# Performance work log

Measured on AMD Instinct MI355X. Metric: run time of the kernel, lower is better.

The kernel has to match this reference:

```python
import jax, jax.numpy as jnp
import numpy as np

MODES = 16
WIDTH = 64
DEPTH = 4
MLP = 128


def spectral_conv(x, w_cplx):
    # x: [B, C, H, W] float32; w_cplx: [C, C, m1, m2] complex64
    B, C, H, W = x.shape
    x_ft = jnp.fft.rfft2(x)  # [B, C, H, W//2+1] complex
    m1, m2 = MODES, MODES
    low = jnp.einsum('bixy,ioxy->boxy', x_ft[:, :, :m1, :m2], w_cplx)
    out_ft = jnp.zeros((B, C, H, W // 2 + 1), dtype=jnp.complex64)
    out_ft = out_ft.at[:, :, :m1, :m2].set(low)
    return jnp.fft.irfft2(out_ft, s=(H, W)).astype(x.dtype)


def conv1x1(x, w, b):
    # x: [B,Cin,H,W], w: [Cout,Cin], b: [Cout]
    return jnp.einsum('bihw,oi->bohw', x, w) + b[None, :, None, None]


def setup_inputs() -> dict:
    key = jax.random.key(0)
    ks = jax.random.split(key, 4 + 4 * DEPTH)
    inp = {}
    inp['x'] = jax.random.normal(ks[0], (8, 3, 256, 256), dtype=jnp.float32)
    inp['fc0_w'] = jax.random.normal(ks[1], (WIDTH, 3), dtype=jnp.float32) * 0.1
    inp['fc0_b'] = jnp.zeros((WIDTH,), dtype=jnp.float32)
    scale = 1.0 / (WIDTH * WIDTH)
    sw_re, sw_im, ww, wb = [], [], [], []
    for i in range(DEPTH):
        k1, k2, k3 = jax.random.split(ks[4 + i], 3)
        sw_re.append(scale * jax.random.uniform(k1, (WIDTH, WIDTH, MODES, MODES), dtype=jnp.float32))
        sw_im.append(scale * jax.random.uniform(k2, (WIDTH, WIDTH, MODES, MODES), dtype=jnp.float32))
        ww.append(jax.random.normal(k3, (WIDTH, WIDTH), dtype=jnp.float32) * 0.05)
        wb.append(jnp.zeros((WIDTH,), dtype=jnp.float32))
    inp['spec_w_re'] = jnp.stack(sw_re)  # [D, C, C, m1, m2]
    inp['spec_w_im'] = jnp.stack(sw_im)
    inp['w_w'] = jnp.stack(ww)           # [D, C, C]
    inp['w_b'] = jnp.stack(wb)           # [D, C]
    inp['fc1_w'] = jax.random.normal(ks[2], (MLP, WIDTH), dtype=jnp.float32) * 0.05
    inp['fc1_b'] = jnp.zeros((MLP,), dtype=jnp.float32)
    inp['fc2_w'] = jax.random.normal(ks[3], (3, MLP), dtype=jnp.float32) * 0.05
    inp['fc2_b'] = jnp.zeros((3,), dtype=jnp.float32)
    return inp


def reference(x, fc0_w, fc0_b, spec_w_re, spec_w_im, w_w, w_b, fc1_w, fc1_b, fc2_w, fc2_b):
    # Dropout is identity in eval mode.
    h = conv1x1(x, fc0_w, fc0_b)  # [B, WIDTH, H, W]
    for i in range(DEPTH):
        w_cplx = spec_w_re[i] + 1j * spec_w_im[i]
        x1 = spectral_conv(h, w_cplx)
        x2 = conv1x1(h, w_w[i], w_b[i])
        h = jax.nn.relu(x1 + x2)
    h = jnp.transpose(h, (0, 2, 3, 1))  # [B, H, W, WIDTH]
    h = jax.nn.relu(jnp.einsum('bhwc,mc->bhwm', h, fc1_w) + fc1_b)
    h = jnp.einsum('bhwm,om->bhwo', h, fc2_w) + fc2_b
    return jnp.transpose(h, (0, 3, 1, 2))  # [B, 3, H, W]
```

## Files before the change

### kernel.cpp

```cpp
#include <hip/hip_runtime.h>

#define Hd 256
#define Wd 256
#define HW 65536
#define C 64
#define B 8
#define M 16
#define NDEPTH 4
#define NMLP 128

typedef __attribute__((ext_vector_type(8))) __bf16 bf16x8;
typedef __attribute__((ext_vector_type(4))) float f32x4;

__device__ inline void bar_lgkm() {
    asm volatile("s_waitcnt lgkmcnt(0)" ::: "memory");
    __builtin_amdgcn_s_barrier();
}

__device__ inline void split_pack8(const float* v, uint4& hq, uint4& lq) {
    unsigned hw[4], lw[4];
#pragma unroll
    for (int i = 0; i < 4; ++i) {
        float a = v[2 * i], bb = v[2 * i + 1];
        unsigned ua = __float_as_uint(a);
        unsigned ha = (ua + 0x7fffu + ((ua >> 16) & 1u)) & 0xffff0000u;
        float ra = a - __uint_as_float(ha);
        unsigned ural = __float_as_uint(ra);
        unsigned la = (ural + 0x7fffu + ((ural >> 16) & 1u)) >> 16;
        unsigned ub = __float_as_uint(bb);
        unsigned hb = (ub + 0x7fffu + ((ub >> 16) & 1u)) & 0xffff0000u;
        float rb = bb - __uint_as_float(hb);
        unsigned urbl = __float_as_uint(rb);
        unsigned lb = (urbl + 0x7fffu + ((urbl >> 16) & 1u)) >> 16;
        hw[i] = (ha >> 16) | (hb & 0xffff0000u);
        lw[i] = la | (lb << 16);
    }
    hq = make_uint4(hw[0], hw[1], hw[2], hw[3]);
    lq = make_uint4(lw[0], lw[1], lw[2], lw[3]);
}

__device__ inline void split1(float s, ushort& h, ushort& l) {
    unsigned ua = __float_as_uint(s);
    unsigned ha = (ua + 0x7fffu + ((ua >> 16) & 1u)) & 0xffff0000u;
    float r = s - __uint_as_float(ha);
    unsigned ur = __float_as_uint(r);
    h = (ushort)(ha >> 16);
    l = (ushort)((ur + 0x7fffu + ((ur >> 16) & 1u)) >> 16);
}

__device__ inline uint4 pack8(const unsigned* v) {
    uint4 r;
    r.x = v[0] | (v[1] << 16);
    r.y = v[2] | (v[3] << 16);
    r.z = v[4] | (v[5] << 16);
    r.w = v[6] | (v[7] << 16);
    return r;
}


__global__ void k_table(float2* __restrict__ tab) {
    int t = threadIdx.x;
    double a = (6.283185307179586476925286766559 / 256.0) * (double)t;
    tab[t] = make_float2((float)cos(a), (float)sin(a));
}

__global__ void k_prep0(const float2* __restrict__ tab, const float* __restrict__ fc1w,
                        const float* __restrict__ ww, float* __restrict__ trig,
                        uint4* __restrict__ trigs_h, uint4* __restrict__ trigs_l,
                        uint4* __restrict__ wws_h, uint4* __restrict__ wws_l,
                        uint4* __restrict__ w1s_h, uint4* __restrict__ w1s_l) {
    int blk = blockIdx.x, t = threadIdx.x;
    if (blk < 32) {
        int k = blk & 15;
        float2 e = tab[(k * t) & 255];
        trig[blk * 256 + t] = (blk < 16) ? e.x : e.y;
    } else if (blk < 36) {
        int idx = (blk - 32) * 256 + t;
        int kc = idx >> 8, x = idx & 255;
        float v[8];
#pragma unroll
        for (int j = 0; j < 8; ++j) {
            int row = kc * 8 + j;
            float2 e = tab[((row & 15) * x) & 255];
            v[j] = (row < 16) ? e.x : e.y;
        }
        uint4 hq, lq; split_pack8(v, hq, lq);
        trigs_h[idx] = hq; trigs_l[idx] = lq;
    } else if (blk < 44) {
        int idx = (blk - 36) * 256 + t;
        int o = idx & 63, kc = (idx >> 6) & 3, ph = (idx >> 8) & 1, d = idx >> 9;
        float v[8];
#pragma unroll
        for (int j = 0; j < 8; ++j)
            v[j] = ww[d * 4096 + o * 64 + ph * 32 + kc * 8 + j];
        uint4 hq, lq; split_pack8(v, hq, lq);
        wws_h[idx] = hq; wws_l[idx] = lq;
    } else {
        int idx = (blk - 44) * 256 + t;
        int m = idx & 127, kc = (idx >> 7) & 3, ph = idx >> 9;
        float v[8];
#pragma unroll
        for (int j = 0; j < 8; ++j)
            v[j] = fc1w[m * 64 + ph * 32 + kc * 8 + j];
        uint4 hq, lq; split_pack8(v, hq, lq);
        w1s_h[idx] = hq; w1s_l[idx] = lq;
    }
}

__global__ void k_prep_et(const float2* __restrict__ tab,
                          uint4* __restrict__ ETh, uint4* __restrict__ ETl) {
    int c = blockIdx.x * 256 + threadIdx.x;
    if (c >= 1024) return;
    int ph = c >> 7, kc = (c >> 5) & 3, m = c & 31;
    float v[8];
#pragma unroll
    for (int j = 0; j < 8; ++j) {
        int y = ph * 32 + kc * 8 + j;
        float2 e = tab[((m & 15) * y) & 255];
        v[j] = (m < 16) ? e.x : -e.y;
    }
    uint4 hq, lq;
    split_pack8(v, hq, lq);
    ETh[c] = hq; ETl[c] = lq;
}

__global__ void k_fc0(const float* __restrict__ x, const float* __restrict__ w,
                      const float* __restrict__ bias,
                      ushort* __restrict__ hs_h, ushort* __restrict__ hs_l) {
    int gp = blockIdx.x * 256 + threadIdx.x;
    int b = gp >> 13, pg = gp & 8191;
    int pix0 = pg * 8;
    float xv[3][8];
#pragma unroll
    for (int ch = 0; ch < 3; ++ch) {
        float4 a = *(const float4*)(x + (size_t)(b * 3 + ch) * HW + pix0);
        float4 c4 = *(const float4*)(x + (size_t)(b * 3 + ch) * HW + pix0 + 4);
        xv[ch][0] = a.x; xv[ch][1] = a.y; xv[ch][2] = a.z; xv[ch][3] = a.w;
        xv[ch][4] = c4.x; xv[ch][5] = c4.y; xv[ch][6] = c4.z; xv[ch][7] = c4.w;
    }
    for (int o = 0; o < C; ++o) {
        float w0 = w[o * 3 + 0], w1 = w[o * 3 + 1], w2 = w[o * 3 + 2], bv = bias[o];
        float v[8];
#pragma unroll
        for (int j = 0; j < 8; ++j)
            v[j] = fmaf(w0, xv[0][j], fmaf(w1, xv[1][j], fmaf(w2, xv[2][j], bv)));
        uint4 hq, lq; split_pack8(v, hq, lq);
        *(uint4*)(hs_h + (size_t)(b * 64 + o) * HW + pix0) = hq;
        *(uint4*)(hs_l + (size_t)(b * 64 + o) * HW + pix0) = lq;
    }
}

__global__ __launch_bounds__(256, 4)
void k_fwd_y(const ushort* __restrict__ hs_h, const ushort* __restrict__ hs_l,
             const uint4* __restrict__ ETh, const uint4* __restrict__ ETl,
             float* __restrict__ T1F) {
    int blk = blockIdx.x;
    int xh = blk & 1, bc = blk >> 1;
    int x0 = xh * 128;
    int t = threadIdx.x;
    int w = t >> 6, l = t & 63;
    int lr = l & 15, lq = l >> 4;
    const ushort* pH = hs_h + (size_t)bc * HW + x0 + w * 32 + lr;
    const ushort* pL = hs_l + (size_t)bc * HW + x0 + w * 32 + lr;
    f32x4 acc[2][2];
#pragma unroll
    for (int u = 0; u < 2; ++u)
#pragma unroll
        for (int xt = 0; xt < 2; ++xt) {
            acc[u][xt][0] = 0.f; acc[u][xt][1] = 0.f;
            acc[u][xt][2] = 0.f; acc[u][xt][3] = 0.f;
        }
    unsigned h0[2][8], l0[2][8], h1[2][8], l1[2][8];
    auto loadp = [&](unsigned hv[2][8], unsigned lv[2][8], int ph) {
#pragma unroll
        for (int xt = 0; xt < 2; ++xt)
#pragma unroll
            for (int j = 0; j < 8; ++j) {
                int off = (ph * 32 + lq * 8 + j) * 256 + xt * 16;
                hv[xt][j] = pH[off];
                lv[xt][j] = pL[off];
            }
    };
    loadp(h0, l0, 0);
#pragma unroll
    for (int ph = 0; ph < 8; ++ph) {
        unsigned (*ch)[8] = (ph & 1) ? h1 : h0;
        unsigned (*cl)[8] = (ph & 1) ? l1 : l0;
        unsigned (*nh)[8] = (ph & 1) ? h0 : h1;
        unsigned (*nl)[8] = (ph & 1) ? l0 : l1;
        if (ph < 7) loadp(nh, nl, ph + 1);
        bf16x8 Ah[2], Al[2];
#pragma unroll
        for (int u = 0; u < 2; ++u) {
            int ci = ph * 128 + lq * 32 + u * 16 + lr;
            Ah[u] = __builtin_bit_cast(bf16x8, ETh[ci]);
            Al[u] = __builtin_bit_cast(bf16x8, ETl[ci]);
        }
#pragma unroll
        for (int xt = 0; xt < 2; ++xt) {
            bf16x8 Bh = __builtin_bit_cast(bf16x8, pack8(ch[xt]));
            bf16x8 Bl = __builtin_bit_cast(bf16x8, pack8(cl[xt]));
#pragma unroll
            for (int u = 0; u < 2; ++u) {
                acc[u][xt] = __builtin_amdgcn_mfma_f32_16x16x32_bf16(Ah[u], Bh, acc[u][xt], 0, 0, 0);
                acc[u][xt] = __builtin_amdgcn_mfma_f32_16x16x32_bf16(Ah[u], Bl, acc[u][xt], 0, 0, 0);
                acc[u][xt] = __builtin_amdgcn_mfma_f32_16x16x32_bf16(Al[u], Bh, acc[u][xt], 0, 0, 0);
            }
        }
    }
#pragma unroll
    for (int u = 0; u < 2; ++u)
#pragma unroll
        for (int xt = 0; xt < 2; ++xt)
#pragma unroll
            for (int g = 0; g < 4; ++g)
                T1F[(size_t)bc * 8192 + (u * 16 + lq * 4 + g) * 256 + x0 + w * 32 + xt * 16 + lr] =
                    acc[u][xt][g];
}

__global__ __launch_bounds__(256, 2)
void k_fwd_x(const float* __restrict__ T1F, const float* __restrict__ trig,
             float2* __restrict__ X) {
    __shared__ float sT[32 * 260];
    __shared__ float sG[32 * 260];
    int bc = blockIdx.x, t = threadIdx.x;
#pragma unroll
    for (int p = 0; p < 8; ++p) {
        int f = t + p * 256;
        int row = f >> 6, seg = f & 63;
        ((float4*)(sT + row * 260))[seg] = *(const float4*)(T1F + (size_t)bc * 8192 + f * 4);
        ((float4*)(sG + row * 260))[seg] = *(const float4*)(trig + row * 256 + seg * 4);
    }
    __syncthreads();
    int ky = t >> 4, kx = t & 15;
    const float* Tr = sT + ky * 260;
    const float* Ti = sT + (16 + ky) * 260;
    const float* Cs = sG + kx * 260;
    const float* Sn = sG + (16 + kx) * 260;
    float xr0 = 0.f, xi0 = 0.f, xr1 = 0.f, xi1 = 0.f;
    for (int q = 0; q < 64; q += 2) {
        float4 tr = *(const float4*)(Tr + q * 4);
        float4 ti = *(const float4*)(Ti + q * 4);
        float4 cs = *(const float4*)(Cs + q * 4);
        float4 sn = *(const float4*)(Sn + q * 4);
        xr0 = fmaf(tr.x, cs.x, xr0); xr0 = fmaf(ti.x, sn.x, xr0);
        xi0 = fmaf(ti.x, cs.x, xi0); xi0 = fmaf(-tr.x, sn.x, xi0);
        xr0 = fmaf(tr.y, cs.y, xr0); xr0 = fmaf(ti.y, sn.y, xr0);
        xi0 = fmaf(ti.y, cs.y, xi0); xi0 = fmaf(-tr.y, sn.y, xi0);
        xr0 = fmaf(tr.z, cs.z, xr0); xr0 = fmaf(ti.z, sn.z, xr0);
        xi0 = fmaf(ti.z, cs.z, xi0); xi0 = fmaf(-tr.z, sn.z, xi0);
        xr0 = fmaf(tr.w, cs.w, xr0); xr0 = fmaf(ti.w, sn.w, xr0);
        xi0 = fmaf(ti.w, cs.w, xi0); xi0 = fmaf(-tr.w, sn.w, xi0);
        float4 tr1 = *(const float4*)(Tr + q * 4 + 4);
        float4 ti1 = *(const float4*)(Ti + q * 4 + 4);
        float4 cs1 = *(const float4*)(Cs + q * 4 + 4);
        float4 sn1 = *(const float4*)(Sn + q * 4 + 4);
        xr1 = fmaf(tr1.x, cs1.x, xr1); xr1 = fmaf(ti1.x, sn1.x, xr1);
        xi1 = fmaf(ti1.x, cs1.x, xi1); xi1 = fmaf(-tr1.x, sn1.x, xi1);
        xr1 = fmaf(tr1.y, cs1.y, xr1); xr1 = fmaf(ti1.y, sn1.y, xr1);
        xi1 = fmaf(ti1.y, cs1.y, xi1); xi1 = fmaf(-tr1.y, sn1.y, xi1);
        xr1 = fmaf(tr1.z, cs1.z, xr1); xr1 = fmaf(ti1.z, sn1.z, xr1);
        xi1 = fmaf(ti1.z, cs1.z, xi1); xi1 = fmaf(-tr1.z, sn1.z, xi1);
        xr1 = fmaf(tr1.w, cs1.w, xr1); xr1 = fmaf(ti1.w, sn1.w, xr1);
        xi1 = fmaf(ti1.w, cs1.w, xi1); xi1 = fmaf(-tr1.w, sn1.w, xi1);
    }
    X[bc * 256 + t] = make_float2(xr0 + xr1, xi0 + xi1);
}

__global__ __launch_bounds__(256, 2)
void k_mix(const float2* __restrict__ X, const float* __restrict__ wre,
           const float* __restrict__ wim, float2* __restrict__ Y) {
    int o = blockIdx.x >> 2;
    int bq = blockIdx.x & 3;
    int m = threadIdx.x;
    int b0 = bq * 2, b1 = bq * 2 + 1;
    float yr0 = 0.f, yi0 = 0.f, yr1 = 0.f, yi1 = 0.f;
    for (int i = 0; i < C; ++i) {
        float wr = wre[(i * C + o) * 256 + m];
        float wi = wim[(i * C + o) * 256 + m];
        float2 x0 = X[(b0 * C + i) * 256 + m];
        float2 x1 = X[(b1 * C + i) * 256 + m];
        yr0 = fmaf(x0.x, wr, fmaf(-x0.y, wi, yr0));
        yi0 = fmaf(x0.x, wi, fmaf(x0.y, wr, yi0));
        yr1 = fmaf(x1.x, wr, fmaf(-x1.y, wi, yr1));
        yi1 = fmaf(x1.x, wi, fmaf(x1.y, wr, yi1));
    }
    Y[(b0 * C + o) * 256 + m] = make_float2(yr0, yi0);
    Y[(b1 * C + o) * 256 + m] = make_float2(yr1, yi1);
}

__global__ __launch_bounds__(256, 2)
void k_invy(const float2* __restrict__ Y, const float2* __restrict__ tab,
            float* __restrict__ Gq) {
    __shared__ float2 st[256];
    int blk = blockIdx.x;
    int yt = blk & 15, pg = (blk >> 4) & 3, b = blk >> 6;
    int t = threadIdx.x;
    st[t] = tab[t];
    int o = t & 63, kx = pg * 4 + (t >> 6);
    __syncthreads();
    float sc = (kx == 0 ? 1.0f : 2.0f) * (1.0f / 65536.0f);
    float yr[16], yi[16];
    const float2* yp = Y + (size_t)(b * 64 + o) * 256 + kx;
#pragma unroll
    for (int ky = 0; ky < 16; ++ky) {
        float2 v = yp[ky * 16];
        yr[ky] = v.x * sc;
        yi[ky] = v.y * sc;
    }
    int y0 = yt * 16;
    for (int yy = 0; yy < 16; ++yy) {
        int y = y0 + yy;
        float re = 0.f, im = 0.f;
#pragma unroll
        for (int ky = 0; ky < 16; ++ky) {
            float2 e = st[(ky * y) & 255];
            re = fmaf(yr[ky], e.x, re);
            re = fmaf(-yi[ky], e.y, re);
            im = fmaf(yr[ky], e.y, im);
            im = fmaf(yi[ky], e.x, im);
        }
        float* gp = Gq + (size_t)(b * 256 + y) * 32 * 64 + o;
        gp[kx * 64] = re;
        gp[(16 + kx) * 64] = -im;
    }
}

__global__ __launch_bounds__(256, 4)
void k_final(ushort* __restrict__ hs_h, ushort* __restrict__ hs_l,
             const float* __restrict__ Gq,
             const uint4* __restrict__ wws_h, const uint4* __restrict__ wws_l,
             const float* __restrict__ wb,
             const uint4* __restrict__ trigs_h, const uint4* __restrict__ trigs_l) {
    __shared__ uint4 smem[2560];
    uint4* sH0h = smem;
    uint4* sH0l = smem + 512;
    uint4* sH1h = smem + 1024;
    uint4* sH1l = smem + 1536;
    uint4* sGh  = smem + 2048;
    uint4* sGl  = smem + 2304;
    int blk = blockIdx.x;
    int xq = blk & 1, y = (blk >> 1) & 255, b = blk >> 9;
    int x0 = xq * 128;
    int t = threadIdx.x;
    int os = t & 63, q = t >> 6;
    int w = t >> 6, l = t & 63;
    int lr = l & 15, lq = l >> 4;
    int xs = t & 127, half = t >> 7;
    f32x4 acc[8];
    {
        int ob = w * 16 + lq * 4;
        f32x4 ini;
        ini[0] = wb[ob]; ini[1] = wb[ob + 1]; ini[2] = wb[ob + 2]; ini[3] = wb[ob + 3];
#pragma unroll
        for (int xt = 0; xt < 8; ++xt) acc[xt] = ini;
    }
    float gv[8];
    {
        const float* gsrc = Gq + ((size_t)(b * 256 + y) * 32 + q * 8) * 64 + os;
#pragma unroll
        for (int kk = 0; kk < 8; ++kk) gv[kk] = gsrc[kk * 64];
    }
    uint4 A0h = wws_h[lq * 64 + w * 16 + lr];
    uint4 A0l = wws_l[lq * 64 + w * 16 + lr];
    uint4 A1h = wws_h[(4 + lq) * 64 + w * 16 + lr];
    uint4 A1l = wws_l[(4 + lq) * 64 + w * 16 + lr];
    size_t hb0 = (size_t)(b * 64 + half * 16) * HW + y * 256 + x0 + xs;
    unsigned hv[16], lv[16];
#pragma unroll
    for (int j = 0; j < 16; ++j) {
        hv[j] = hs_h[hb0 + (size_t)j * HW];
        lv[j] = hs_l[hb0 + (size_t)j * HW];
    }
    {
        uint4 ghq, glq; split_pack8(gv, ghq, glq);
        sGh[q * 64 + os] = ghq; sGl[q * 64 + os] = glq;
    }
#pragma unroll
    for (int c2 = 0; c2 < 2; ++c2) {
        int cell = (half * 2 + c2) * 128 + xs;
        sH0h[cell] = pack8(hv + c2 * 8);
        sH0l[cell] = pack8(lv + c2 * 8);
    }
    unsigned hv1[16], lv1[16];
    size_t hb1 = hb0 + (size_t)32 * HW;
#pragma unroll
    for (int j = 0; j < 16; ++j) {
        hv1[j] = hs_h[hb1 + (size_t)j * HW];
        lv1[j] = hs_l[hb1 + (size_t)j * HW];
    }
    bar_lgkm();
#pragma unroll
    for (int xt = 0; xt < 8; ++xt) {
        bf16x8 Bh = __builtin_bit_cast(bf16x8, sH0h[lq * 128 + xt * 16 + lr]);
        bf16x8 Bl = __builtin_bit_cast(bf16x8, sH0l[lq * 128 + xt * 16 + lr]);
        bf16x8 Ah = __builtin_bit_cast(bf16x8, A0h);
        bf16x8 Al = __builtin_bit_cast(bf16x8, A0l);
        acc[xt] = __builtin_amdgcn_mfma_f32_16x16x32_bf16(Ah, Bh, acc[xt], 0, 0, 0);
        acc[xt] = __builtin_amdgcn_mfma_f32_16x16x32_bf16(Ah, Bl, acc[xt], 0, 0, 0);
        acc[xt] = __builtin_amdgcn_mfma_f32_16x16x32_bf16(Al, Bh, acc[xt], 0, 0, 0);
    }
#pragma unroll
    for (int c2 = 0; c2 < 2; ++c2) {
        int cell = (half * 2 + c2) * 128 + xs;
        sH1h[cell] = pack8(hv1 + c2 * 8);
        sH1l[cell] = pack8(lv1 + c2 * 8);
    }
    bar_lgkm();
#pragma unroll
    for (int xt = 0; xt < 8; ++xt) {
        bf16x8 Bh = __builtin_bit_cast(bf16x8, sH1h[lq * 128 + xt * 16 + lr]);
        bf16x8 Bl = __builtin_bit_cast(bf16x8, sH1l[lq * 128 + xt * 16 + lr]);
        bf16x8 Ah = __builtin_bit_cast(bf16x8, A1h);
        bf16x8 Al = __builtin_bit_cast(bf16x8, A1l);
        acc[xt] = __builtin_amdgcn_mfma_f32_16x16x32_bf16(Ah, Bh, acc[xt], 0, 0, 0);
        acc[xt] = __builtin_amdgcn_mfma_f32_16x16x32_bf16(Ah, Bl, acc[xt], 0, 0, 0);
        acc[xt] = __builtin_amdgcn_mfma_f32_16x16x32_bf16(Al, Bh, acc[xt], 0, 0, 0);
    }
    {
        bf16x8 Ah = __builtin_bit_cast(bf16x8, sGh[lq * 64 + w * 16 + lr]);
        bf16x8 Al = __builtin_bit_cast(bf16x8, sGl[lq * 64 + w * 16 + lr]);
#pragma unroll
        for (int xt = 0; xt < 8; ++xt) {
            bf16x8 Bh = __builtin_bit_cast(bf16x8, trigs_h[lq * 256 + x0 + xt * 16 + lr]);
            bf16x8 Bl = __builtin_bit_cast(bf16x8, trigs_l[lq * 256 + x0 + xt * 16 + lr]);
            acc[xt] = __builtin_amdgcn_mfma_f32_16x16x32_bf16(Ah, Bh, acc[xt], 0, 0, 0);
            acc[xt] = __builtin_amdgcn_mfma_f32_16x16x32_bf16(Ah, Bl, acc[xt], 0, 0, 0);
            acc[xt] = __builtin_amdgcn_mfma_f32_16x16x32_bf16(Al, Bh, acc[xt], 0, 0, 0);
        }
    }
    __syncthreads();
    ushort* eh = (ushort*)smem;
    ushort* el = (ushort*)(smem + 1024);
#pragma unroll
    for (int xt = 0; xt < 8; ++xt)
#pragma unroll
        for (int g = 0; g < 4; ++g) {
            int o = w * 16 + lq * 4 + g;
            float r = fmaxf(acc[xt][g], 0.f);
            ushort hh, ll; split1(r, hh, ll);
            eh[o * 128 + xt * 16 + lr] = hh;
            el[o * 128 + xt * 16 + lr] = ll;
        }
    __syncthreads();
#pragma unroll
    for (int p = 0; p < 4; ++p) {
        int f = t + p * 256;
        int o = f >> 4, seg = f & 15;
        size_t base = (size_t)(b * 64 + o) * HW + y * 256 + x0;
        *(uint4*)(hs_h + base + seg * 8) = smem[f];
        *(uint4*)(hs_l + base + seg * 8) = smem[1024 + f];
    }
}

__global__ __launch_bounds__(256, 3)
void k_fc12(const ushort* __restrict__ hs_h, const ushort* __restrict__ hs_l,
            const uint4* __restrict__ w1s_h, const uint4* __restrict__ w1s_l,
            const float* __restrict__ b1, const float* __restrict__ w2,
            const float* __restrict__ b2, float* __restrict__ out) {
    __shared__ uint4 sH0h[512], sH0l[512], sH1h[512], sH1l[512];
    int blk = blockIdx.x;
    int xq = blk & 1, y = (blk >> 1) & 255, b = blk >> 9;
    int x0 = xq * 128;
    int t = threadIdx.x;
    int w = t >> 6, l = t & 63;
    int lr = l & 15, lq = l >> 4;
    int mb = w * 32;
    int xs = t & 127, half = t >> 7;
    f32x4 acc[2][8];
#pragma unroll
    for (int u = 0; u < 2; ++u) {
        int m0 = mb + u * 16 + lq * 4;
        f32x4 ini;
        ini[0] = b1[m0]; ini[1] = b1[m0 + 1]; ini[2] = b1[m0 + 2]; ini[3] = b1[m0 + 3];
#pragma unroll
        for (int xt = 0; xt < 8; ++xt) acc[u][xt] = ini;
    }
    uint4 a0h[2], a0l[2], a1h[2], a1l[2];
#pragma unroll
    for (int u = 0; u < 2; ++u) {
        a0h[u] = w1s_h[lq * 128 + mb + u * 16 + lr];
        a0l[u] = w1s_l[lq * 128 + mb + u * 16 + lr];
        a1h[u] = w1s_h[(4 + lq) * 128 + mb + u * 16 + lr];
        a1l[u] = w1s_l[(4 + lq) * 128 + mb + u * 16 + lr];
    }
    size_t hb0 = (size_t)(b * 64 + half * 16) * HW + y * 256 + x0 + xs;
    unsigned hv[16], lv[16];
#pragma unroll
    for (int j = 0; j < 16; ++j) {
        hv[j] = hs_h[hb0 + (size_t)j * HW];
        lv[j] = hs_l[hb0 + (size_t)j * HW];
    }
#pragma unroll
    for (int c2 = 0; c2 < 2; ++c2) {
        int cell = (half * 2 + c2) * 128 + xs;
        sH0h[cell] = pack8(hv + c2 * 8);
        sH0l[cell] = pack8(lv + c2 * 8);
    }
    unsigned hv1[16], lv1[16];
    size_t hb1 = hb0 + (size_t)32 * HW;
#pragma unroll
    for (int j = 0; j < 16; ++j) {
        hv1[j] = hs_h[hb1 + (size_t)j * HW];
        lv1[j] = hs_l[hb1 + (size_t)j * HW];
    }
    bar_lgkm();
#pragma unroll
    for (int xt = 0; xt < 8; ++xt) {
        bf16x8 Bh = __builtin_bit_cast(bf16x8, sH0h[lq * 128 + xt * 16 + lr]);
        bf16x8 Bl = __builtin_bit_cast(bf16x8, sH0l[lq * 128 + xt * 16 + lr]);
#pragma unroll
        for (int u = 0; u < 2; ++u) {
            bf16x8 Ah = __builtin_bit_cast(bf16x8, a0h[u]);
            bf16x8 Al = __builtin_bit_cast(bf16x8, a0l[u]);
            acc[u][xt] = __builtin_amdgcn_mfma_f32_16x16x32_bf16(Ah, Bh, acc[u][xt], 0, 0, 0);
            acc[u][xt] = __builtin_amdgcn_mfma_f32_16x16x32_bf16(Ah, Bl, acc[u][xt], 0, 0, 0);
            acc[u][xt] = __builtin_amdgcn_mfma_f32_16x16x32_bf16(Al, Bh, acc[u][xt], 0, 0, 0);
        }
    }
#pragma unroll
    for (int c2 = 0; c2 < 2; ++c2) {
        int cell = (half * 2 + c2) * 128 + xs;
        sH1h[cell] = pack8(hv1 + c2 * 8);
        sH1l[cell] = pack8(lv1 + c2 * 8);
    }
    bar_lgkm();
#pragma unroll
    for (int xt = 0; xt < 8; ++xt) {
        bf16x8 Bh = __builtin_bit_cast(bf16x8, sH1h[lq * 128 + xt * 16 + lr]);
        bf16x8 Bl = __builtin_bit_cast(bf16x8, sH1l[lq * 128 + xt * 16 + lr]);
#pragma unroll
        for (int u = 0; u < 2; ++u) {
            bf16x8 Ah = __builtin_bit_cast(bf16x8, a1h[u]);
            bf16x8 Al = __builtin_bit_cast(bf16x8, a1l[u]);
            acc[u][xt] = __builtin_amdgcn_mfma_f32_16x16x32_bf16(Ah, Bh, acc[u][xt], 0, 0, 0);
            acc[u][xt] = __builtin_amdgcn_mfma_f32_16x16x32_bf16(Ah, Bl, acc[u][xt], 0, 0, 0);
            acc[u][xt] = __builtin_amdgcn_mfma_f32_16x16x32_bf16(Al, Bh, acc[u][xt], 0, 0, 0);
        }
    }
    float pj[3][8];
#pragma unroll
    for (int j = 0; j < 3; ++j)
#pragma unroll
        for (int xt = 0; xt < 8; ++xt) pj[j][xt] = 0.f;
#pragma unroll
    for (int u = 0; u < 2; ++u)
#pragma unroll
        for (int g = 0; g < 4; ++g) {
            int m = mb + u * 16 + lq * 4 + g;
            float w20 = w2[m], w21 = w2[NMLP + m], w22 = w2[2 * NMLP + m];
#pragma unroll
            for (int xt = 0; xt < 8; ++xt) {
                float r = fmaxf(acc[u][xt][g], 0.f);
                pj[0][xt] = fmaf(w20, r, pj[0][xt]);
                pj[1][xt] = fmaf(w21, r, pj[1][xt]);
                pj[2][xt] = fmaf(w22, r, pj[2][xt]);
            }
        }
#pragma unroll
    for (int j = 0; j < 3; ++j)
#pragma unroll
        for (int xt = 0; xt < 8; ++xt) {
            float v = pj[j][xt];
            v += __shfl_xor(v, 16);
            v += __shfl_xor(v, 32);
            pj[j][xt] = v;
        }
    float* part = (float*)sH0h;
    if (lq == 0) {
#pragma unroll
        for (int j = 0; j < 3; ++j)
#pragma unroll
            for (int xt = 0; xt < 8; ++xt)
                part[(w * 3 + j) * 128 + xt * 16 + lr] = pj[j][xt];
    }
    __syncthreads();
#pragma unroll
    for (int r = 0; r < 2; ++r) {
        int idx = t + r * 256;
        if (idx < 384) {
            int j = idx >> 7, xx = idx & 127;
            float s = b2[j];
#pragma unroll
            for (int ww2 = 0; ww2 < 4; ++ww2) s += part[(ww2 * 3 + j) * 128 + xx];
            out[(size_t)(b * 3 + j) * HW + y * 256 + x0 + xx] = s;
        }
    }
}

extern "C" void kernel_launch(void* const* d_in, const int* in_sizes, int n_in,
                              void* d_out, int out_size, void* d_ws, size_t ws_size,
                              hipStream_t stream) {
    const float* x     = (const float*)d_in[0];
    const float* fc0_w = (const float*)d_in[1];
    const float* fc0_b = (const float*)d_in[2];
    const float* swre  = (const float*)d_in[3];
    const float* swim  = (const float*)d_in[4];
    const float* ww    = (const float*)d_in[5];
    const float* wb    = (const float*)d_in[6];
    const float* fc1w  = (const float*)d_in[7];
    const float* fc1b  = (const float*)d_in[8];
    const float* fc2w  = (const float*)d_in[9];
    const float* fc2b  = (const float*)d_in[10];

    float* ws = (float*)d_ws;
    float2* tab     = (float2*)ws;
    ushort* hs_h    = (ushort*)(ws + 512);
    ushort* hs_l    = (ushort*)(ws + 512 + 16777216);
    float*  T1F     = ws + 33554944;
    float2* X       = (float2*)(ws + 37749248);
    float2* Y       = (float2*)(ws + 38011392);
    float*  Gq      = ws + 38273536;
    float*  trig    = ws + 42467840;
    uint4*  trigs_h = (uint4*)(ws + 42476032);
    uint4*  trigs_l = (uint4*)(ws + 42480128);
    uint4*  wws_h   = (uint4*)(ws + 42484224);
    uint4*  wws_l   = (uint4*)(ws + 42492416);
    uint4*  w1s_h   = (uint4*)(ws + 42500608);
    uint4*  w1s_l   = (uint4*)(ws + 42504704);
    uint4*  ETh     = (uint4*)(ws + 42508800);
    uint4*  ETl     = (uint4*)(ws + 42512896);

    k_table<<<dim3(1), dim3(256), 0, stream>>>(tab);
    k_prep0<<<dim3(48), dim3(256), 0, stream>>>(tab, fc1w, ww, trig,
                                                trigs_h, trigs_l, wws_h, wws_l,
                                                w1s_h, w1s_l);
    k_prep_et<<<dim3(4), dim3(256), 0, stream>>>(tab, ETh, ETl);
    k_fc0<<<dim3(256), dim3(256), 0, stream>>>(x, fc0_w, fc0_b, hs_h, hs_l);

    for (int d = 0; d < NDEPTH; ++d) {
        k_fwd_y<<<dim3(1024), dim3(256), 0, stream>>>(hs_h, hs_l, ETh, ETl, T1F);
        k_fwd_x<<<dim3(512), dim3(256), 0, stream>>>(T1F, trig, X);
        k_mix<<<dim3(256), dim3(256), 0, stream>>>(X, swre + (size_t)d * C * C * 256,
                                                   swim + (size_t)d * C * C * 256, Y);
        k_invy<<<dim3(512), dim3(256), 0, stream>>>(Y, tab, Gq);
        k_final<<<dim3(4096), dim3(256), 0, stream>>>(hs_h, hs_l, Gq,
                                                      wws_h + (size_t)d * 512,
                                                      wws_l + (size_t)d * 512,
                                                      wb + d * C, trigs_h, trigs_l);
    }
    k_fc12<<<dim3(4096), dim3(256), 0, stream>>>(hs_h, hs_l, w1s_h, w1s_l,
                                                 fc1b, fc2w, fc2b, (float*)d_out);
}
```

Baseline: 693.8 us.

## Fuse final spectral layer with fc1/fc2 head and trim k_final LDS

The last depth layer's output update is fused with the fc1/fc2 MLP head, so that layer's activations go from registers into LDS and straight into the fc1 MFMAs. This avoids writing the hs_h/hs_l tensors to global memory and reading them back in a separate k_fc12 launch. k_final also builds the G operand in registers instead of staging it through LDS, cutting LDS from 40KB to 32KB and raising the occupancy hint to 5 blocks. It adds an XOR swizzle on the epilogue LDS writes to reduce bank conflicts. The fused kernel carries more accumulator registers, which may limit its occupancy.

```diff
diff --git a/kernel.cpp b/kernel.cpp
--- a/kernel.cpp
+++ b/kernel.cpp
@@ -326,24 +326,21 @@
     }
 }
 
-__global__ __launch_bounds__(256, 4)
+__global__ __launch_bounds__(256, 5)
 void k_final(ushort* __restrict__ hs_h, ushort* __restrict__ hs_l,
              const float* __restrict__ Gq,
              const uint4* __restrict__ wws_h, const uint4* __restrict__ wws_l,
              const float* __restrict__ wb,
              const uint4* __restrict__ trigs_h, const uint4* __restrict__ trigs_l) {
-    __shared__ uint4 smem[2560];
+    __shared__ uint4 smem[2048];
     uint4* sH0h = smem;
     uint4* sH0l = smem + 512;
     uint4* sH1h = smem + 1024;
     uint4* sH1l = smem + 1536;
-    uint4* sGh  = smem + 2048;
-    uint4* sGl  = smem + 2304;
     int blk = blockIdx.x;
     int xq = blk & 1, y = (blk >> 1) & 255, b = blk >> 9;
     int x0 = xq * 128;
     int t = threadIdx.x;
-    int os = t & 63, q = t >> 6;
     int w = t >> 6, l = t & 63;
     int lr = l & 15, lq = l >> 4;
     int xs = t & 127, half = t >> 7;
@@ -357,7 +354,7 @@
     }
     float gv[8];
     {
-        const float* gsrc = Gq + ((size_t)(b * 256 + y) * 32 + q * 8) * 64 + os;
+        const float* gsrc = Gq + ((size_t)(b * 256 + y) * 32 + lq * 8) * 64 + w * 16 + lr;
 #pragma unroll
         for (int kk = 0; kk < 8; ++kk) gv[kk] = gsrc[kk * 64];
     }
@@ -371,10 +368,6 @@
     for (int j = 0; j < 16; ++j) {
         hv[j] = hs_h[hb0 + (size_t)j * HW];
         lv[j] = hs_l[hb0 + (size_t)j * HW];
-    }
-    {
-        uint4 ghq, glq; split_pack8(gv, ghq, glq);
-        sGh[q * 64 + os] = ghq; sGl[q * 64 + os] = glq;
     }
 #pragma unroll
     for (int c2 = 0; c2 < 2; ++c2) {
@@ -418,8 +411,9 @@
         acc[xt] = __builtin_amdgcn_mfma_f32_16x16x32_bf16(Al, Bh, acc[xt], 0, 0, 0);
     }
     {
-        bf16x8 Ah = __builtin_bit_cast(bf16x8, sGh[lq * 64 + w * 16 + lr]);
-        bf16x8 Al = __builtin_bit_cast(bf16x8, sGl[lq * 64 + w * 16 + lr]);
+        uint4 gh4, gl4; split_pack8(gv, gh4, gl4);
+        bf16x8 Ah = __builtin_bit_cast(bf16x8, gh4);
+        bf16x8 Al = __builtin_bit_cast(bf16x8, gl4);
 #pragma unroll
         for (int xt = 0; xt < 8; ++xt) {
             bf16x8 Bh = __builtin_bit_cast(bf16x8, trigs_h[lq * 256 + x0 + xt * 16 + lr]);
@@ -432,6 +426,7 @@
     __syncthreads();
     ushort* eh = (ushort*)smem;
     ushort* el = (ushort*)(smem + 1024);
+    int swz = lq * 40;
 #pragma unroll
     for (int xt = 0; xt < 8; ++xt)
 #pragma unroll
@@ -439,103 +434,168 @@
             int o = w * 16 + lq * 4 + g;
             float r = fmaxf(acc[xt][g], 0.f);
             ushort hh, ll; split1(r, hh, ll);
-            eh[o * 128 + xt * 16 + lr] = hh;
-            el[o * 128 + xt * 16 + lr] = ll;
+            int col = (xt * 16 + lr) ^ swz;
+            eh[o * 128 + col] = hh;
+            el[o * 128 + col] = ll;
         }
     __syncthreads();
 #pragma unroll
     for (int p = 0; p < 4; ++p) {
         int f = t + p * 256;
         int o = f >> 4, seg = f & 15;
+        int ko = ((o >> 2) & 3) * 40;
+        int cb = (seg * 8) ^ ko;
         size_t base = (size_t)(b * 64 + o) * HW + y * 256 + x0;
-        *(uint4*)(hs_h + base + seg * 8) = smem[f];
-        *(uint4*)(hs_l + base + seg * 8) = smem[1024 + f];
+        *(uint4*)(hs_h + base + seg * 8) = *(uint4*)(eh + o * 128 + cb);
+        *(uint4*)(hs_l + base + seg * 8) = *(uint4*)(el + o * 128 + cb);
     }
 }
 
 __global__ __launch_bounds__(256, 3)
-void k_fc12(const ushort* __restrict__ hs_h, const ushort* __restrict__ hs_l,
-            const uint4* __restrict__ w1s_h, const uint4* __restrict__ w1s_l,
-            const float* __restrict__ b1, const float* __restrict__ w2,
-            const float* __restrict__ b2, float* __restrict__ out) {
-    __shared__ uint4 sH0h[512], sH0l[512], sH1h[512], sH1l[512];
+void k_final_fc(const ushort* __restrict__ hs_h, const ushort* __restrict__ hs_l,
+                const float* __restrict__ Gq,
+                const uint4* __restrict__ wws_h, const uint4* __restrict__ wws_l,
+                const float* __restrict__ wb,
+                const uint4* __restrict__ trigs_h, const uint4* __restrict__ trigs_l,
+                const uint4* __restrict__ w1s_h, const uint4* __restrict__ w1s_l,
+                const float* __restrict__ b1, const float* __restrict__ w2,
+                const float* __restrict__ b2, float* __restrict__ out) {
+    __shared__ uint4 smem[2048];
+    uint4* sH0h = smem;
+    uint4* sH0l = smem + 512;
+    uint4* sH1h = smem + 1024;
+    uint4* sH1l = smem + 1536;
     int blk = blockIdx.x;
     int xq = blk & 1, y = (blk >> 1) & 255, b = blk >> 9;
     int x0 = xq * 128;
     int t = threadIdx.x;
     int w = t >> 6, l = t & 63;
     int lr = l & 15, lq = l >> 4;
+    int xs = t & 127, half = t >> 7;
+    f32x4 acc[8];
+    {
+        int ob = w * 16 + lq * 4;
+        f32x4 ini;
+        ini[0] = wb[ob]; ini[1] = wb[ob + 1]; ini[2] = wb[ob + 2]; ini[3] = wb[ob + 3];
+#pragma unroll
+        for (int xt = 0; xt < 8; ++xt) acc[xt] = ini;
+    }
+    float gv[8];
+    {
+        const float* gsrc = Gq + ((size_t)(b * 256 + y) * 32 + lq * 8) * 64 + w * 16 + lr;
+#pragma unroll
+        for (int kk = 0; kk < 8; ++kk) gv[kk] = gsrc[kk * 64];
+    }
+    uint4 A0h = wws_h[lq * 64 + w * 16 + lr];
+    uint4 A0l = wws_l[lq * 64 + w * 16 + lr];
+    uint4 A1h = wws_h[(4 + lq) * 64 + w * 16 + lr];
+    uint4 A1l = wws_l[(4 + lq) * 64 + w * 16 + lr];
+    size_t hb0 = (size_t)(b * 64 + half * 16) * HW + y * 256 + x0 + xs;
+    unsigned hv[16], lv[16];
+#pragma unroll
+    for (int j = 0; j < 16; ++j) {
+        hv[j] = hs_h[hb0 + (size_t)j * HW];
+        lv[j] = hs_l[hb0 + (size_t)j * HW];
+    }
+#pragma unroll
+    for (int c2 = 0; c2 < 2; ++c2) {
+        int cell = (half * 2 + c2) * 128 + xs;
+        sH0h[cell] = pack8(hv + c2 * 8);
+        sH0l[cell] = pack8(lv + c2 * 8);
+    }
+    unsigned hv1[16], lv1[16];
+    size_t hb1 = hb0 + (size_t)32 * HW;
+#pragma unroll
+    for (int j = 0; j < 16; ++j) {
+        hv1[j] = hs_h[hb1 + (size_t)j * HW];
+        lv1[j] = hs_l[hb1 + (size_t)j * HW];
+    }
+    bar_lgkm();
+#pragma unroll
+    for (int xt = 0; xt < 8; ++xt) {
+        bf16x8 Bh = __builtin_bit_cast(bf16x8, sH0h[lq * 128 + xt * 16 + lr]);
+        bf16x8 Bl = __builtin_bit_cast(bf16x8, sH0l[lq * 128 + xt * 16 + lr]);
+        bf16x8 Ah = __builtin_bit_cast(bf16x8, A0h);
+        bf16x8 Al = __builtin_bit_cast(bf16x8, A0l);
+        acc[xt] = __builtin_amdgcn_mfma_f32_16x16x32_bf16(Ah, Bh, acc[xt], 0, 0, 0);
+        acc[xt] = __builtin_amdgcn_mfma_f32_16x16x32_bf16(Ah, Bl, acc[xt], 0, 0, 0);
+        acc[xt] = __builtin_amdgcn_mfma_f32_16x16x32_bf16(Al, Bh, acc[xt], 0, 0, 0);
+    }
+#pragma unroll
+    for (int c2 = 0; c2 < 2; ++c2) {
+        int cell = (half * 2 + c2) * 128 + xs;
+        sH1h[cell] = pack8(hv1 + c2 * 8);
+        sH1l[cell] = pack8(lv1 + c2 * 8);
+    }
+    bar_lgkm();
+#pragma unroll
+    for (int xt = 0; xt < 8; ++xt) {
+        bf16x8 Bh = __builtin_bit_cast(bf16x8, sH1h[lq * 128 + xt * 16 + lr]);
+        bf16x8 Bl = __builtin_bit_cast(bf16x8, sH1l[lq * 128 + xt * 16 + lr]);
+        bf16x8 Ah = __builtin_bit_cast(bf16x8, A1h);
+        bf16x8 Al = __builtin_bit_cast(bf16x8, A1l);
+        acc[xt] = __builtin_amdgcn_mfma_f32_16x16x32_bf16(Ah, Bh, acc[xt], 0, 0, 0);
+        acc[xt] = __builtin_amdgcn_mfma_f32_16x16x32_bf16(Ah, Bl, acc[xt], 0, 0, 0);
+        acc[xt] = __builtin_amdgcn_mfma_f32_16x16x32_bf16(Al, Bh, acc[xt], 0, 0, 0);
+    }
+    {
+        uint4 gh4, gl4; split_pack8(gv, gh4, gl4);
+        bf16x8 Ah = __builtin_bit_cast(bf16x8, gh4);
+        bf16x8 Al = __builtin_bit_cast(bf16x8, gl4);
+#pragma unroll
+        for (int xt = 0; xt < 8; ++xt) {
+            bf16x8 Bh = __builtin_bit_cast(bf16x8, trigs_h[lq * 256 + x0 + xt * 16 + lr]);
+            bf16x8 Bl = __builtin_bit_cast(bf16x8, trigs_l[lq * 256 + x0 + xt * 16 + lr]);
+            acc[xt] = __builtin_amdgcn_mfma_f32_16x16x32_bf16(Ah, Bh, acc[xt], 0, 0, 0);
+            acc[xt] = __builtin_amdgcn_mfma_f32_16x16x32_bf16(Ah, Bl, acc[xt], 0, 0, 0);
+            acc[xt] = __builtin_amdgcn_mfma_f32_16x16x32_bf16(Al, Bh, acc[xt], 0, 0, 0);
+        }
+    }
+    __syncthreads();
+    ushort* ch16 = (ushort*)smem;
+    ushort* cl16 = (ushort*)(smem + 1024);
+#pragma unroll
+    for (int xt = 0; xt < 8; ++xt)
+#pragma unroll
+        for (int g = 0; g < 4; ++g) {
+            int o = w * 16 + lq * 4 + g;
+            float r = fmaxf(acc[xt][g], 0.f);
+            ushort hh, ll; split1(r, hh, ll);
+            int ci = ((o >> 3) * 128 + xt * 16 + lr) * 8 + (o & 7);
+            ch16[ci] = hh;
+            cl16[ci] = ll;
+        }
+    __syncthreads();
+    uint4* cells_h = smem;
+    uint4* cells_l = smem + 1024;
     int mb = w * 32;
-    int xs = t & 127, half = t >> 7;
-    f32x4 acc[2][8];
+    f32x4 acc2[2][8];
 #pragma unroll
     for (int u = 0; u < 2; ++u) {
         int m0 = mb + u * 16 + lq * 4;
         f32x4 ini;
         ini[0] = b1[m0]; ini[1] = b1[m0 + 1]; ini[2] = b1[m0 + 2]; ini[3] = b1[m0 + 3];
 #pragma unroll
-        for (int xt = 0; xt < 8; ++xt) acc[u][xt] = ini;
-    }
-    uint4 a0h[2], a0l[2], a1h[2], a1l[2];
-#pragma unroll
-    for (int u = 0; u < 2; ++u) {
-        a0h[u] = w1s_h[lq * 128 + mb + u * 16 + lr];
-        a0l[u] = w1s_l[lq * 128 + mb + u * 16 + lr];
-        a1h[u] = w1s_h[(4 + lq) * 128 + mb + u * 16 + lr];
-        a1l[u] = w1s_l[(4 + lq) * 128 + mb + u * 16 + lr];
-    }
-    size_t hb0 = (size_t)(b * 64 + half * 16) * HW + y * 256 + x0 + xs;
-    unsigned hv[16], lv[16];
-#pragma unroll
-    for (int j = 0; j < 16; ++j) {
-        hv[j] = hs_h[hb0 + (size_t)j * HW];
-        lv[j] = hs_l[hb0 + (size_t)j * HW];
-    }
-#pragma unroll
-    for (int c2 = 0; c2 < 2; ++c2) {
-        int cell = (half * 2 + c2) * 128 + xs;
-        sH0h[cell] = pack8(hv + c2 * 8);
-        sH0l[cell] = pack8(lv + c2 * 8);
-    }
-    unsigned hv1[16], lv1[16];
-    size_t hb1 = hb0 + (size_t)32 * HW;
-#pragma unroll
-    for (int j = 0; j < 16; ++j) {
-        hv1[j] = hs_h[hb1 + (size_t)j * HW];
-        lv1[j] = hs_l[hb1 + (size_t)j * HW];
-    }
-    bar_lgkm();
-#pragma unroll
-    for (int xt = 0; xt < 8; ++xt) {
-        bf16x8 Bh = __builtin_bit_cast(bf16x8, sH0h[lq * 128 + xt * 16 + lr]);
-        bf16x8 Bl = __builtin_bit_cast(bf16x8, sH0l[lq * 128 + xt * 16 + lr]);
+        for (int xt = 0; xt < 8; ++xt) acc2[u][xt] = ini;
+    }
+#pragma unroll
+    for (int ph = 0; ph < 2; ++ph) {
+        bf16x8 Ah[2], Al[2];
 #pragma unroll
         for (int u = 0; u < 2; ++u) {
-            bf16x8 Ah = __builtin_bit_cast(bf16x8, a0h[u]);
-            bf16x8 Al = __builtin_bit_cast(bf16x8, a0l[u]);
-            acc[u][xt] = __builtin_amdgcn_mfma_f32_16x16x32_bf16(Ah, Bh, acc[u][xt], 0, 0, 0);
-            acc[u][xt] = __builtin_amdgcn_mfma_f32_16x16x32_bf16(Ah, Bl, acc[u][xt], 0, 0, 0);
-            acc[u][xt] = __builtin_amdgcn_mfma_f32_16x16x32_bf16(Al, Bh, acc[u][xt], 0, 0, 0);
-        }
-    }
-#pragma unroll
-    for (int c2 = 0; c2 < 2; ++c2) {
-        int cell = (half * 2 + c2) * 128 + xs;
-        sH1h[cell] = pack8(hv1 + c2 * 8);
-        sH1l[cell] = pack8(lv1 + c2 * 8);
-    }
-    bar_lgkm();
-#pragma unroll
-    for (int xt = 0; xt < 8; ++xt) {
-        bf16x8 Bh = __builtin_bit_cast(bf16x8, sH1h[lq * 128 + xt * 16 + lr]);
-        bf16x8 Bl = __builtin_bit_cast(bf16x8, sH1l[lq * 128 + xt * 16 + lr]);
-#pragma unroll
-        for (int u = 0; u < 2; ++u) {
-            bf16x8 Ah = __builtin_bit_cast(bf16x8, a1h[u]);
-            bf16x8 Al = __builtin_bit_cast(bf16x8, a1l[u]);
-            acc[u][xt] = __builtin_amdgcn_mfma_f32_16x16x32_bf16(Ah, Bh, acc[u][xt], 0, 0, 0);
-            acc[u][xt] = __builtin_amdgcn_mfma_f32_16x16x32_bf16(Ah, Bl, acc[u][xt], 0, 0, 0);
-            acc[u][xt] = __builtin_amdgcn_mfma_f32_16x16x32_bf16(Al, Bh, acc[u][xt], 0, 0, 0);
+            Ah[u] = __builtin_bit_cast(bf16x8, w1s_h[(ph * 4 + lq) * 128 + mb + u * 16 + lr]);
+            Al[u] = __builtin_bit_cast(bf16x8, w1s_l[(ph * 4 + lq) * 128 + mb + u * 16 + lr]);
+        }
+#pragma unroll
+        for (int xt = 0; xt < 8; ++xt) {
+            bf16x8 Bh = __builtin_bit_cast(bf16x8, cells_h[(ph * 4 + lq) * 128 + xt * 16 + lr]);
+            bf16x8 Bl = __builtin_bit_cast(bf16x8, cells_l[(ph * 4 + lq) * 128 + xt * 16 + lr]);
+#pragma unroll
+            for (int u = 0; u < 2; ++u) {
+                acc2[u][xt] = __builtin_amdgcn_mfma_f32_16x16x32_bf16(Ah[u], Bh, acc2[u][xt], 0, 0, 0);
+                acc2[u][xt] = __builtin_amdgcn_mfma_f32_16x16x32_bf16(Ah[u], Bl, acc2[u][xt], 0, 0, 0);
+                acc2[u][xt] = __builtin_amdgcn_mfma_f32_16x16x32_bf16(Al[u], Bh, acc2[u][xt], 0, 0, 0);
+            }
         }
     }
     float pj[3][8];
@@ -551,7 +611,7 @@
             float w20 = w2[m], w21 = w2[NMLP + m], w22 = w2[2 * NMLP + m];
 #pragma unroll
             for (int xt = 0; xt < 8; ++xt) {
-                float r = fmaxf(acc[u][xt][g], 0.f);
+                float r = fmaxf(acc2[u][xt][g], 0.f);
                 pj[0][xt] = fmaf(w20, r, pj[0][xt]);
                 pj[1][xt] = fmaf(w21, r, pj[1][xt]);
                 pj[2][xt] = fmaf(w22, r, pj[2][xt]);
@@ -566,7 +626,8 @@
             v += __shfl_xor(v, 32);
             pj[j][xt] = v;
         }
-    float* part = (float*)sH0h;
+    __syncthreads();
+    float* part = (float*)smem;
     if (lq == 0) {
 #pragma unroll
         for (int j = 0; j < 3; ++j)
@@ -634,11 +695,18 @@
         k_mix<<<dim3(256), dim3(256), 0, stream>>>(X, swre + (size_t)d * C * C * 256,
                                                    swim + (size_t)d * C * C * 256, Y);
         k_invy<<<dim3(512), dim3(256), 0, stream>>>(Y, tab, Gq);
-        k_final<<<dim3(4096), dim3(256), 0, stream>>>(hs_h, hs_l, Gq,
-                                                      wws_h + (size_t)d * 512,
-                                                      wws_l + (size_t)d * 512,
-                                                      wb + d * C, trigs_h, trigs_l);
-    }
-    k_fc12<<<dim3(4096), dim3(256), 0, stream>>>(hs_h, hs_l, w1s_h, w1s_l,
-                                                 fc1b, fc2w, fc2b, (float*)d_out);
-}
+        if (d < NDEPTH - 1) {
+            k_final<<<dim3(4096), dim3(256), 0, stream>>>(hs_h, hs_l, Gq,
+                                                          wws_h + (size_t)d * 512,
+                                                          wws_l + (size_t)d * 512,
+                                                          wb + d * C, trigs_h, trigs_l);
+        } else {
+            k_final_fc<<<dim3(4096), dim3(256), 0, stream>>>(hs_h, hs_l, Gq,
+                                                             wws_h + (size_t)d * 512,
+                                                             wws_l + (size_t)d * 512,
+                                                             wb + d * C, trigs_h, trigs_l,
+                                                             w1s_h, w1s_l, fc1b, fc2w,
+                                                             fc2b, (float*)d_out);
+        }
+    }
+}
```

Result: faster. 666.2 us (-4.0%).
